# Optimization experiments

Hardware: AMD Instinct MI355X
Metric: run time of the kernel (lower is better)

The kernel has to match this reference:

```python
import jax, jax.numpy as jnp
import numpy as np

DIM = 1024
HEADS = 16
D_HEAD = 64
INNER = HEADS * D_HEAD  # 1024
CTX_DIM = 768
FF_INNER = 4 * DIM  # 4096
EPS = 1e-5
SCALE = D_HEAD ** -0.5


def _layer_norm(x, g, b):
    m = jnp.mean(x, axis=-1, keepdims=True)
    v = jnp.mean(jnp.square(x - m), axis=-1, keepdims=True)
    return (x - m) * jax.lax.rsqrt(v + EPS) * g + b


def _attention(x, ctx, wq, wk, wv, wo, bo):
    B, S, _ = x.shape
    T = ctx.shape[1]
    # project and split heads -> [B, H, S, Dh]
    q = (x @ wq).reshape(B, S, HEADS, D_HEAD).transpose(0, 2, 1, 3)
    k = (ctx @ wk).reshape(B, T, HEADS, D_HEAD).transpose(0, 2, 1, 3)
    v = (ctx @ wv).reshape(B, T, HEADS, D_HEAD).transpose(0, 2, 1, 3)
    attn = jnp.einsum('bhid,bhjd->bhij', q, k) * SCALE
    attn = jax.nn.softmax(attn, axis=-1)
    out = jnp.einsum('bhij,bhjd->bhid', attn, v)  # [B, H, S, Dh]
    out = out.transpose(0, 2, 1, 3).reshape(B, S, INNER)
    return out @ wo + bo


def setup_inputs() -> dict:
    key = jax.random.key(0)
    ks = jax.random.split(key, 20)
    rn = lambda k, shape, s=0.02: jax.random.normal(k, shape, dtype=jnp.float32) * s
    inp = {
        'hidden_states': jax.random.normal(ks[0], (4, 2048, DIM), dtype=jnp.float32),
        'context': jax.random.normal(ks[1], (4, 77, CTX_DIM), dtype=jnp.float32),
        # self-attention
        'wq1': rn(ks[2], (DIM, INNER)), 'wk1': rn(ks[3], (DIM, INNER)),
        'wv1': rn(ks[4], (DIM, INNER)),
        'wo1': rn(ks[5], (INNER, DIM)), 'bo1': jnp.zeros((DIM,), jnp.float32),
        # cross-attention (k/v from context dim 768)
        'wq2': rn(ks[6], (DIM, INNER)), 'wk2': rn(ks[7], (CTX_DIM, INNER)),
        'wv2': rn(ks[8], (CTX_DIM, INNER)),
        'wo2': rn(ks[9], (INNER, DIM)), 'bo2': jnp.zeros((DIM,), jnp.float32),
        # GEGLU feed-forward
        'w_ff1': rn(ks[10], (DIM, 2 * FF_INNER)), 'b_ff1': jnp.zeros((2 * FF_INNER,), jnp.float32),
        'w_ff2': rn(ks[11], (FF_INNER, DIM)), 'b_ff2': jnp.zeros((DIM,), jnp.float32),
        # layer norms
        'ln1_g': jnp.ones((DIM,), jnp.float32), 'ln1_b': jnp.zeros((DIM,), jnp.float32),
        'ln2_g': jnp.ones((DIM,), jnp.float32), 'ln2_b': jnp.zeros((DIM,), jnp.float32),
        'ln3_g': jnp.ones((DIM,), jnp.float32), 'ln3_b': jnp.zeros((DIM,), jnp.float32),
    }
    return inp


def reference(hidden_states, context, wq1, wk1, wv1, wo1, bo1,
              wq2, wk2, wv2, wo2, bo2, w_ff1, b_ff1, w_ff2, b_ff2,
              ln1_g, ln1_b, ln2_g, ln2_b, ln3_g, ln3_b):
    # self-attention, pre-norm residual
    h = hidden_states
    h = h + _attention(_layer_norm(h, ln1_g, ln1_b), _layer_norm(h, ln1_g, ln1_b),
                       wq1, wk1, wv1, wo1, bo1)
    # cross-attention
    h = h + _attention(_layer_norm(h, ln2_g, ln2_b), context,
                       wq2, wk2, wv2, wo2, bo2)
    # GEGLU feed-forward
    x = _layer_norm(h, ln3_g, ln3_b) @ w_ff1 + b_ff1
    lin, gate = jnp.split(x, 2, axis=2)
    h = h + (lin * jax.nn.gelu(gate)) @ w_ff2 + b_ff2
    return h
```

## Files before the change

### kernel.cpp

```cpp
#include <hip/hip_runtime.h>

#define DIMM 1024
#define NHEADS 16
#define DHEAD 64
#define BATCH 4
#define SEQ 2048
#define TCTX 77
#define CTXD 768
#define FFI 4096

typedef float f32x4 __attribute__((ext_vector_type(4)));
typedef __bf16 bf16x8 __attribute__((ext_vector_type(8)));

__device__ __forceinline__ float bf2f(unsigned short u){
  union { unsigned int i; float f; } c; c.i = ((unsigned int)u) << 16; return c.f;
}
__device__ __forceinline__ unsigned short f2bf(float f){
  union { float f; unsigned int i; } c; c.f = f;
  unsigned int i = c.i;
  return (unsigned short)((i + 0x7fffu + ((i >> 16) & 1u)) >> 16);
}
__device__ __forceinline__ void cp16(const unsigned short* g, unsigned short* l){
  __builtin_amdgcn_global_load_lds(
      (const __attribute__((address_space(1))) unsigned int*)g,
      (__attribute__((address_space(3))) unsigned int*)l, 16, 0, 0);
}

__global__ __launch_bounds__(256) void ln_kernel(const float* __restrict__ x,
                                                 const float* __restrict__ g,
                                                 const float* __restrict__ bb,
                                                 unsigned short* __restrict__ y)
{
  int row = blockIdx.x, tid = threadIdx.x;
  float4 raw = ((const float4*)(x + (size_t)row * DIMM))[tid];
  float v0 = raw.x, v1 = raw.y, v2 = raw.z, v3 = raw.w;
  float s  = v0 + v1 + v2 + v3;
  float sq = v0*v0 + v1*v1 + v2*v2 + v3*v3;
  #pragma unroll
  for (int off = 32; off; off >>= 1){ s += __shfl_xor(s, off); sq += __shfl_xor(sq, off); }
  __shared__ float sm[8];
  int wave = tid >> 6, lane = tid & 63;
  if (lane == 0){ sm[wave] = s; sm[4 + wave] = sq; }
  __syncthreads();
  s  = sm[0] + sm[1] + sm[2] + sm[3];
  sq = sm[4] + sm[5] + sm[6] + sm[7];
  float mean = s * (1.f / DIMM);
  float var  = sq * (1.f / DIMM) - mean * mean;
  float rstd = rsqrtf(var + 1e-5f);
  float4 gr = ((const float4*)g)[tid];
  float4 br = ((const float4*)bb)[tid];
  ushort4 o;
  o.x = f2bf((v0 - mean) * rstd * gr.x + br.x);
  o.y = f2bf((v1 - mean) * rstd * gr.y + br.y);
  o.z = f2bf((v2 - mean) * rstd * gr.z + br.z);
  o.w = f2bf((v3 - mean) * rstd * gr.w + br.w);
  ((ushort4*)(y + (size_t)row * DIMM))[tid] = o;
}

__global__ __launch_bounds__(256) void wt_kernel(const float* __restrict__ in,
                                                 unsigned short* __restrict__ out,
                                                 int K, int N)
{
  __shared__ float t[32][33];
  int tx = threadIdx.x & 31, ty = threadIdx.x >> 5;
  int k0 = blockIdx.y * 32, n0 = blockIdx.x * 32;
  #pragma unroll
  for (int i = 0; i < 4; i++)
    t[ty + i * 8][tx] = in[(size_t)(k0 + ty + i * 8) * N + n0 + tx];
  __syncthreads();
  #pragma unroll
  for (int i = 0; i < 4; i++)
    out[(size_t)(n0 + ty + i * 8) * K + k0 + tx] = f2bf(t[tx][ty + i * 8]);
}

#define CTXE (TCTX * BATCH * CTXD)
__global__ __launch_bounds__(256) void ctxcvt_kernel(const float* __restrict__ in,
                                                     unsigned short* __restrict__ out)
{
  int e = (blockIdx.x * 256 + threadIdx.x) * 4;
  float4 v;
  if (e < CTXE) v = *(const float4*)(in + e);
  else { v.x = 0.f; v.y = 0.f; v.z = 0.f; v.w = 0.f; }
  ushort4 o; o.x = f2bf(v.x); o.y = f2bf(v.y); o.z = f2bf(v.z); o.w = f2bf(v.w);
  *(ushort4*)(out + e) = o;
}

template<int RESF, int CF32>
__global__ __launch_bounds__(256) void gemm_bt(
    const unsigned short* __restrict__ A, int lda,
    const unsigned short* __restrict__ Bt, int ldb,
    const float* __restrict__ bias, const void* __restrict__ resv,
    void* __restrict__ Cv, int ldc,
    int M, int N, int K)
{
  __shared__ __align__(16) unsigned short As[128][64];
  __shared__ __align__(16) unsigned short Bs[128][64];
  int tid = threadIdx.x;
  int n0 = blockIdx.x * 128, row0 = blockIdx.y * 128;
  int wave = tid >> 6, lane = tid & 63, quad = lane >> 4, l16 = lane & 15;
  int wm = (wave >> 1) * 64, wn = (wave & 1) * 64;
  int wrow = wave * 32;
  int lrow = lane >> 3, lgrp = lane & 7;
  int gcol = ((lgrp ^ lrow) * 8);

  f32x4 acc[4][4];
  #pragma unroll
  for (int mt = 0; mt < 4; mt++)
    #pragma unroll
    for (int nt = 0; nt < 4; nt++) acc[mt][nt] = 0.f;

  for (int k0 = 0; k0 < K; k0 += 64) {
    const unsigned short* ga = A  + (size_t)(row0 + wrow + lrow) * lda + k0 + gcol;
    const unsigned short* gb = Bt + (size_t)(n0  + wrow + lrow) * ldb + k0 + gcol;
    #pragma unroll
    for (int i = 0; i < 4; i++){
      cp16(ga + (size_t)(8 * i) * lda, &As[wrow + 8 * i][0]);
      cp16(gb + (size_t)(8 * i) * ldb, &Bs[wrow + 8 * i][0]);
    }
    __syncthreads();
    #pragma unroll
    for (int kc = 0; kc < 2; kc++){
      bf16x8 af[4], bf[4];
      #pragma unroll
      for (int mt = 0; mt < 4; mt++){
        int R = wm + mt * 16 + l16;
        af[mt] = *(const bf16x8*)&As[R][((kc * 4 + quad) ^ (R & 7)) * 8];
      }
      #pragma unroll
      for (int nt = 0; nt < 4; nt++){
        int R = wn + nt * 16 + l16;
        bf[nt] = *(const bf16x8*)&Bs[R][((kc * 4 + quad) ^ (R & 7)) * 8];
      }
      #pragma unroll
      for (int mt = 0; mt < 4; mt++)
        #pragma unroll
        for (int nt = 0; nt < 4; nt++)
          acc[mt][nt] = __builtin_amdgcn_mfma_f32_16x16x32_bf16(af[mt], bf[nt], acc[mt][nt], 0, 0, 0);
    }
    __syncthreads();
  }

  #pragma unroll
  for (int nt = 0; nt < 4; nt++){
    int c = n0 + wn + nt * 16 + l16;
    float bv = bias ? bias[c] : 0.f;
    #pragma unroll
    for (int mt = 0; mt < 4; mt++){
      int rbase = row0 + wm + mt * 16 + quad * 4;
      #pragma unroll
      for (int rr = 0; rr < 4; rr++){
        int r = rbase + rr;
        if (r < M) {
          float val = acc[mt][nt][rr] + bv;
          size_t idx = (size_t)r * ldc + c;
          if (RESF) val += ((const float*)resv)[idx];
          if (CF32) ((float*)Cv)[idx] = val;
          else      ((unsigned short*)Cv)[idx] = f2bf(val);
        }
      }
    }
  }
}

__global__ __launch_bounds__(256) void ff1_geglu_bt(
    const unsigned short* __restrict__ A,
    const unsigned short* __restrict__ BtW,
    const float* __restrict__ bias,
    unsigned short* __restrict__ Z, int M)
{
  __shared__ __align__(16) unsigned short As[128][64];
  __shared__ __align__(16) unsigned short BsL[128][64];
  __shared__ __align__(16) unsigned short BsG[128][64];
  int tid = threadIdx.x;
  int n0 = blockIdx.x * 128, row0 = blockIdx.y * 128;
  int wave = tid >> 6, lane = tid & 63, quad = lane >> 4, l16 = lane & 15;
  int wm = (wave >> 1) * 64, wn = (wave & 1) * 64;
  int wrow = wave * 32;
  int lrow = lane >> 3, lgrp = lane & 7;
  int gcol = ((lgrp ^ lrow) * 8);

  f32x4 accL[4][4], accG[4][4];
  #pragma unroll
  for (int mt = 0; mt < 4; mt++)
    #pragma unroll
    for (int nt = 0; nt < 4; nt++){ accL[mt][nt] = 0.f; accG[mt][nt] = 0.f; }

  for (int k0 = 0; k0 < DIMM; k0 += 64) {
    const unsigned short* ga = A   + (size_t)(row0 + wrow + lrow) * DIMM + k0 + gcol;
    const unsigned short* gl = BtW + (size_t)(n0  + wrow + lrow) * DIMM + k0 + gcol;
    const unsigned short* gg = BtW + (size_t)(FFI + n0 + wrow + lrow) * DIMM + k0 + gcol;
    #pragma unroll
    for (int i = 0; i < 4; i++){
      cp16(ga + (size_t)(8 * i) * DIMM, &As[wrow + 8 * i][0]);
      cp16(gl + (size_t)(8 * i) * DIMM, &BsL[wrow + 8 * i][0]);
      cp16(gg + (size_t)(8 * i) * DIMM, &BsG[wrow + 8 * i][0]);
    }
    __syncthreads();
    #pragma unroll
    for (int kc = 0; kc < 2; kc++){
      bf16x8 af[4], b[4];
      #pragma unroll
      for (int mt = 0; mt < 4; mt++){
        int R = wm + mt * 16 + l16;
        af[mt] = *(const bf16x8*)&As[R][((kc * 4 + quad) ^ (R & 7)) * 8];
      }
      #pragma unroll
      for (int nt = 0; nt < 4; nt++){
        int R = wn + nt * 16 + l16;
        b[nt] = *(const bf16x8*)&BsL[R][((kc * 4 + quad) ^ (R & 7)) * 8];
      }
      #pragma unroll
      for (int mt = 0; mt < 4; mt++)
        #pragma unroll
        for (int nt = 0; nt < 4; nt++)
          accL[mt][nt] = __builtin_amdgcn_mfma_f32_16x16x32_bf16(af[mt], b[nt], accL[mt][nt], 0, 0, 0);
      #pragma unroll
      for (int nt = 0; nt < 4; nt++){
        int R = wn + nt * 16 + l16;
        b[nt] = *(const bf16x8*)&BsG[R][((kc * 4 + quad) ^ (R & 7)) * 8];
      }
      #pragma unroll
      for (int mt = 0; mt < 4; mt++)
        #pragma unroll
        for (int nt = 0; nt < 4; nt++)
          accG[mt][nt] = __builtin_amdgcn_mfma_f32_16x16x32_bf16(af[mt], b[nt], accG[mt][nt], 0, 0, 0);
    }
    __syncthreads();
  }

  #pragma unroll
  for (int nt = 0; nt < 4; nt++){
    int c = n0 + wn + nt * 16 + l16;
    float bvL = bias[c];
    float bvG = bias[c + FFI];
    #pragma unroll
    for (int mt = 0; mt < 4; mt++){
      int rbase = row0 + wm + mt * 16 + quad * 4;
      #pragma unroll
      for (int rr = 0; rr < 4; rr++){
        float lin = accL[mt][nt][rr] + bvL;
        float g   = accG[mt][nt][rr] + bvG;
        float y = 0.7978845608028654f * (g + 0.044715f * g * g * g);
        float e = __builtin_amdgcn_exp2f(y * 2.8853900817779268f);
        float t = 1.f - 2.f * __builtin_amdgcn_rcpf(e + 1.f);
        Z[(size_t)(rbase + rr) * FFI + c] = f2bf(lin * 0.5f * g * (1.f + t));
      }
    }
  }
}

__global__ __launch_bounds__(256, 8) void attn_mfma(
    const unsigned short* __restrict__ Q, int ldq,
    const unsigned short* __restrict__ Kb,
    const unsigned short* __restrict__ Vb, int ldkv,
    unsigned short* __restrict__ O,
    int S, int T, float scale)
{
  int tid = threadIdx.x, wave = tid >> 6, lane = tid & 63;
  int quad = lane >> 4, l16 = lane & 15;
  int bh = blockIdx.y, b = bh >> 4, h = bh & 15;
  int qw = blockIdx.x * 64 + wave * 16;

  __shared__ __align__(16) unsigned short Ks[64][64];
  __shared__ __align__(16) unsigned short Vt[64][72];

  float qs = scale * 1.44269504088896f;
  bf16x8 Qf[2];
  #pragma unroll
  for (int kc = 0; kc < 2; kc++){
    const unsigned short* qp = Q + ((size_t)b * S + qw + l16) * ldq
                                 + h * DHEAD + kc * 32 + quad * 8;
    union { float4 v; unsigned short u[8]; } ld; ld.v = *(const float4*)qp;
    union { bf16x8 v; unsigned short u[8]; } sc;
    #pragma unroll
    for (int j = 0; j < 8; j++) sc.u[j] = f2bf(bf2f(ld.u[j]) * qs);
    Qf[kc] = sc.v;
  }

  f32x4 Oacc[4];
  float lp = 0.f;
  #pragma unroll
  for (int nt = 0; nt < 4; nt++) Oacc[nt] = 0.f;

  int lrow = lane >> 3, lgrp = lane & 7;
  int gcol = (lgrp ^ lrow) * 8;

  for (int j0 = 0; j0 < T; j0 += 64){
    bool tail = (j0 + 64 > T);
    if (!tail){
      const unsigned short* gk = Kb + ((size_t)b * T + j0 + wave * 16 + lrow) * ldkv
                                    + h * DHEAD + gcol;
      cp16(gk,                      &Ks[wave * 16 + lrow][0]);
      cp16(gk + (size_t)8 * ldkv,   &Ks[wave * 16 + 8 + lrow][0]);
    } else {
      #pragma unroll
      for (int p = 0; p < 2; p++){
        int key = p * 32 + (tid >> 3);
        int g = tid & 7;
        float4 kv;
        if (j0 + key < T) kv = *(const float4*)(Kb + ((size_t)b * T + j0 + key) * ldkv + h * DHEAD + g * 8);
        else { kv.x = 0.f; kv.y = 0.f; kv.z = 0.f; kv.w = 0.f; }
        *(float4*)&Ks[key][(g ^ (key & 7)) * 8] = kv;
      }
    }
    {
      int j = tid & 63, dbs = (tid >> 6) * 16;
      if (j0 + j < T){
        union { float4 v; unsigned short u[8]; } v1, v2;
        const unsigned short* vp = Vb + ((size_t)b * T + j0 + j) * ldkv + h * DHEAD + dbs;
        v1.v = ((const float4*)vp)[0];
        v2.v = ((const float4*)vp)[1];
        #pragma unroll
        for (int u = 0; u < 8; u++){ Vt[dbs + u][j] = v1.u[u]; Vt[dbs + 8 + u][j] = v2.u[u]; }
      } else {
        #pragma unroll
        for (int u = 0; u < 8; u++){ Vt[dbs + u][j] = 0; Vt[dbs + 8 + u][j] = 0; }
      }
    }
    __syncthreads();

    union pfu { bf16x8 v; __bf16 e[8]; } pf[2];
    {
      f32x4 sT[4];
      #pragma unroll
      for (int nt = 0; nt < 4; nt++){
        sT[nt] = 0.f;
        #pragma unroll
        for (int kc = 0; kc < 2; kc++){
          bf16x8 kf = *(const bf16x8*)&Ks[nt * 16 + l16][((kc * 4 + quad) ^ (l16 & 7)) * 8];
          sT[nt] = __builtin_amdgcn_mfma_f32_16x16x32_bf16(kf, Qf[kc], sT[nt], 0, 0, 0);
        }
      }
      #pragma unroll
      for (int nt = 0; nt < 4; nt++)
        #pragma unroll
        for (int rr = 0; rr < 4; rr++){
          float sv = sT[nt][rr];
          if (tail && (j0 + nt * 16 + quad * 4 + rr) >= T) sv = -1e30f;
          float p = __builtin_amdgcn_exp2f(fminf(sv, 108.f));
          lp += p;
          pf[nt >> 1].e[(nt & 1) * 4 + rr] = (__bf16)p;
        }
    }

    #pragma unroll
    for (int kc = 0; kc < 2; kc++)
      #pragma unroll
      for (int nt = 0; nt < 4; nt++){
        union { bf16x8 v; ushort4 u[2]; } vf;
        vf.u[0] = *(const ushort4*)&Vt[nt * 16 + l16][kc * 32 + quad * 4];
        vf.u[1] = *(const ushort4*)&Vt[nt * 16 + l16][kc * 32 + 16 + quad * 4];
        Oacc[nt] = __builtin_amdgcn_mfma_f32_16x16x32_bf16(pf[kc].v, vf.v, Oacc[nt], 0, 0, 0);
      }
    __syncthreads();
  }

  float l = lp;
  l += __shfl_xor(l, 16);
  l += __shfl_xor(l, 32);
  float inv[4];
  #pragma unroll
  for (int rr = 0; rr < 4; rr++)
    inv[rr] = 1.f / __shfl(l, quad * 4 + rr);
  #pragma unroll
  for (int nt = 0; nt < 4; nt++)
    #pragma unroll
    for (int rr = 0; rr < 4; rr++){
      size_t idx = ((size_t)b * S + qw + quad * 4 + rr) * DIMM
                   + h * DHEAD + nt * 16 + l16;
      O[idx] = f2bf(Oacc[nt][rr] * inv[rr]);
    }
}

extern "C" void kernel_launch(void* const* d_in, const int* in_sizes, int n_in,
                              void* d_out, int out_size, void* d_ws, size_t ws_size,
                              hipStream_t stream)
{
  const float* h0   = (const float*)d_in[0];
  const float* ctx  = (const float*)d_in[1];
  const float* wq1  = (const float*)d_in[2];
  const float* wk1  = (const float*)d_in[3];
  const float* wv1  = (const float*)d_in[4];
  const float* wo1  = (const float*)d_in[5];
  const float* bo1  = (const float*)d_in[6];
  const float* wq2  = (const float*)d_in[7];
  const float* wk2  = (const float*)d_in[8];
  const float* wv2  = (const float*)d_in[9];
  const float* wo2  = (const float*)d_in[10];
  const float* bo2  = (const float*)d_in[11];
  const float* wff1 = (const float*)d_in[12];
  const float* bff1 = (const float*)d_in[13];
  const float* wff2 = (const float*)d_in[14];
  const float* bff2 = (const float*)d_in[15];
  const float* ln1g = (const float*)d_in[16];
  const float* ln1b = (const float*)d_in[17];
  const float* ln2g = (const float*)d_in[18];
  const float* ln2b = (const float*)d_in[19];
  const float* ln3g = (const float*)d_in[20];
  const float* ln3b = (const float*)d_in[21];

  unsigned short* wsp = (unsigned short*)d_ws;
  const size_t RD = (size_t)BATCH * SEQ * DIMM;
  unsigned short* xn  = wsp;
  unsigned short* qkv = wsp + RD;
  unsigned short* ar  = wsp + 4 * RD;
  unsigned short* zb  = qkv;
  float* hres = (float*)d_out;

  const size_t M1 = (size_t)1024 * 1024;
  const int ROWS = BATCH * SEQ;
  const int CROWS = BATCH * TCTX;
  const float scale = 0.125f;
  dim3 blk(256);
  dim3 attn_grid(SEQ / 64, BATCH * NHEADS);

  wt_kernel<<<dim3(32, 32), blk, 0, stream>>>(wq1, ar,          DIMM, DIMM);
  wt_kernel<<<dim3(32, 32), blk, 0, stream>>>(wk1, ar + M1,     DIMM, DIMM);
  wt_kernel<<<dim3(32, 32), blk, 0, stream>>>(wv1, ar + 2 * M1, DIMM, DIMM);
  wt_kernel<<<dim3(32, 32), blk, 0, stream>>>(wo1, ar + 3 * M1, DIMM, DIMM);
  ln_kernel<<<ROWS, blk, 0, stream>>>(h0, ln1g, ln1b, xn);
  gemm_bt<0,0><<<dim3(3072 / 128, ROWS / 128), blk, 0, stream>>>(
      xn, DIMM, ar, DIMM, nullptr, nullptr, qkv, 3072, ROWS, 3072, DIMM);
  attn_mfma<<<attn_grid, blk, 0, stream>>>(qkv, 3072, qkv + 1024, qkv + 2048, 3072, xn, SEQ, SEQ, scale);
  gemm_bt<1,1><<<dim3(DIMM / 128, ROWS / 128), blk, 0, stream>>>(
      xn, DIMM, ar + 3 * M1, DIMM, bo1, h0, hres, DIMM, ROWS, DIMM, DIMM);

  unsigned short* wq2T  = ar;
  unsigned short* wkv2T = ar + M1;
  unsigned short* wo2T  = ar + M1 + (size_t)2048 * CTXD;
  unsigned short* xc    = wo2T + M1;
  wt_kernel<<<dim3(32, 32), blk, 0, stream>>>(wq2, wq2T, DIMM, DIMM);
  wt_kernel<<<dim3(32, 24), blk, 0, stream>>>(wk2, wkv2T, CTXD, DIMM);
  wt_kernel<<<dim3(32, 24), blk, 0, stream>>>(wv2, wkv2T + (size_t)1024 * CTXD, CTXD, DIMM);
  wt_kernel<<<dim3(32, 32), blk, 0, stream>>>(wo2, wo2T, DIMM, DIMM);
  ctxcvt_kernel<<<(384 * CTXD / 4) / 256, blk, 0, stream>>>(ctx, xc);
  ln_kernel<<<ROWS, blk, 0, stream>>>(hres, ln2g, ln2b, xn);
  gemm_bt<0,0><<<dim3(DIMM / 128, ROWS / 128), blk, 0, stream>>>(
      xn, DIMM, wq2T, DIMM, nullptr, nullptr, qkv, DIMM, ROWS, DIMM, DIMM);
  unsigned short* kvc = qkv + RD;
  gemm_bt<0,0><<<dim3(2048 / 128, 3), blk, 0, stream>>>(
      xc, CTXD, wkv2T, CTXD, nullptr, nullptr, kvc, 2048, CROWS, 2048, CTXD);
  attn_mfma<<<attn_grid, blk, 0, stream>>>(qkv, 1024, kvc, kvc + 1024, 2048, xn, SEQ, TCTX, scale);
  gemm_bt<1,1><<<dim3(DIMM / 128, ROWS / 128), blk, 0, stream>>>(
      xn, DIMM, wo2T, DIMM, bo2, hres, hres, DIMM, ROWS, DIMM, DIMM);

  unsigned short* wff1T = ar;
  unsigned short* wff2T = ar + 8 * M1;
  wt_kernel<<<dim3(256, 32),  blk, 0, stream>>>(wff1, wff1T, DIMM, 2 * FFI);
  wt_kernel<<<dim3(32, 128),  blk, 0, stream>>>(wff2, wff2T, FFI, DIMM);
  ln_kernel<<<ROWS, blk, 0, stream>>>(hres, ln3g, ln3b, xn);
  for (int half = 0; half < 2; half++){
    int r0 = half * 4096;
    ff1_geglu_bt<<<dim3(FFI / 128, 4096 / 128), blk, 0, stream>>>(
        xn + (size_t)r0 * DIMM, wff1T, bff1, zb, 4096);
    gemm_bt<1,1><<<dim3(DIMM / 128, 4096 / 128), blk, 0, stream>>>(
        zb, FFI, wff2T, FFI, bff2, hres + (size_t)r0 * DIMM,
        hres + (size_t)r0 * DIMM, DIMM, 4096, DIMM, FFI);
  }
}
```

Measured before the change: 1.022 ms.

## Use 512-thread attention blocks and swizzled V layout for 128-byte fragment reads

The attention kernel now runs 8 waves per block over 128 queries, so each K/V tile loaded into shared memory serves twice as many query rows and per-thread load work halves. V is stored with an XOR-swizzled, MFMA-fragment-friendly layout, so each PV fragment becomes a single 16-byte LDS read instead of two 8-byte reads from a padded transpose. The risks are lower occupancy from larger blocks and that the cp16 destination passes only the row base, which relies on the global_load_lds lane-offset semantics.

```diff
diff --git a/kernel.cpp b/kernel.cpp
--- a/kernel.cpp
+++ b/kernel.cpp
@@ -249,7 +249,7 @@
   }
 }
 
-__global__ __launch_bounds__(256, 8) void attn_mfma(
+__global__ __launch_bounds__(512, 8) void attn_mfma(
     const unsigned short* __restrict__ Q, int ldq,
     const unsigned short* __restrict__ Kb,
     const unsigned short* __restrict__ Vb, int ldkv,
@@ -259,10 +259,10 @@
   int tid = threadIdx.x, wave = tid >> 6, lane = tid & 63;
   int quad = lane >> 4, l16 = lane & 15;
   int bh = blockIdx.y, b = bh >> 4, h = bh & 15;
-  int qw = blockIdx.x * 64 + wave * 16;
+  int qw = blockIdx.x * 128 + wave * 16;
 
   __shared__ __align__(16) unsigned short Ks[64][64];
-  __shared__ __align__(16) unsigned short Vt[64][72];
+  __shared__ __align__(16) unsigned short Vp[64][64];
 
   float qs = scale * 1.44269504088896f;
   bf16x8 Qf[2];
@@ -284,38 +284,31 @@
 
   int lrow = lane >> 3, lgrp = lane & 7;
   int gcol = (lgrp ^ lrow) * 8;
+  int vj = lane;
+  int vchunk = ((vj >> 5) << 2) | ((vj >> 2) & 3);
+  int velem  = (((vj >> 4) & 1) << 2) | (vj & 3);
+  int dbs = wave * 8;
 
   for (int j0 = 0; j0 < T; j0 += 64){
     bool tail = (j0 + 64 > T);
     if (!tail){
-      const unsigned short* gk = Kb + ((size_t)b * T + j0 + wave * 16 + lrow) * ldkv
+      const unsigned short* gk = Kb + ((size_t)b * T + j0 + wave * 8 + lrow) * ldkv
                                     + h * DHEAD + gcol;
-      cp16(gk,                      &Ks[wave * 16 + lrow][0]);
-      cp16(gk + (size_t)8 * ldkv,   &Ks[wave * 16 + 8 + lrow][0]);
+      cp16(gk, &Ks[wave * 8][0]);
     } else {
-      #pragma unroll
-      for (int p = 0; p < 2; p++){
-        int key = p * 32 + (tid >> 3);
-        int g = tid & 7;
-        float4 kv;
-        if (j0 + key < T) kv = *(const float4*)(Kb + ((size_t)b * T + j0 + key) * ldkv + h * DHEAD + g * 8);
-        else { kv.x = 0.f; kv.y = 0.f; kv.z = 0.f; kv.w = 0.f; }
-        *(float4*)&Ks[key][(g ^ (key & 7)) * 8] = kv;
-      }
+      int key = tid >> 3, g = tid & 7;
+      float4 kv;
+      if (j0 + key < T) kv = *(const float4*)(Kb + ((size_t)b * T + j0 + key) * ldkv + h * DHEAD + g * 8);
+      else { kv.x = 0.f; kv.y = 0.f; kv.z = 0.f; kv.w = 0.f; }
+      *(float4*)&Ks[key][(g ^ (key & 7)) * 8] = kv;
     }
     {
-      int j = tid & 63, dbs = (tid >> 6) * 16;
-      if (j0 + j < T){
-        union { float4 v; unsigned short u[8]; } v1, v2;
-        const unsigned short* vp = Vb + ((size_t)b * T + j0 + j) * ldkv + h * DHEAD + dbs;
-        v1.v = ((const float4*)vp)[0];
-        v2.v = ((const float4*)vp)[1];
-        #pragma unroll
-        for (int u = 0; u < 8; u++){ Vt[dbs + u][j] = v1.u[u]; Vt[dbs + 8 + u][j] = v2.u[u]; }
-      } else {
-        #pragma unroll
-        for (int u = 0; u < 8; u++){ Vt[dbs + u][j] = 0; Vt[dbs + 8 + u][j] = 0; }
-      }
+      union { float4 v; unsigned short u[8]; } vv;
+      if (j0 + vj < T) vv.v = *(const float4*)(Vb + ((size_t)b * T + j0 + vj) * ldkv + h * DHEAD + dbs);
+      else { vv.v.x = 0.f; vv.v.y = 0.f; vv.v.z = 0.f; vv.v.w = 0.f; }
+      #pragma unroll
+      for (int u = 0; u < 8; u++)
+        Vp[dbs + u][((vchunk ^ u) << 3) | velem] = vv.u[u];
     }
     __syncthreads();
 
@@ -347,10 +340,9 @@
     for (int kc = 0; kc < 2; kc++)
       #pragma unroll
       for (int nt = 0; nt < 4; nt++){
-        union { bf16x8 v; ushort4 u[2]; } vf;
-        vf.u[0] = *(const ushort4*)&Vt[nt * 16 + l16][kc * 32 + quad * 4];
-        vf.u[1] = *(const ushort4*)&Vt[nt * 16 + l16][kc * 32 + 16 + quad * 4];
-        Oacc[nt] = __builtin_amdgcn_mfma_f32_16x16x32_bf16(pf[kc].v, vf.v, Oacc[nt], 0, 0, 0);
+        int R = nt * 16 + l16;
+        bf16x8 vf = *(const bf16x8*)&Vp[R][((kc * 4 + quad) ^ (R & 7)) * 8];
+        Oacc[nt] = __builtin_amdgcn_mfma_f32_16x16x32_bf16(pf[kc].v, vf, Oacc[nt], 0, 0, 0);
       }
     __syncthreads();
   }
@@ -412,7 +404,8 @@
   const int CROWS = BATCH * TCTX;
   const float scale = 0.125f;
   dim3 blk(256);
-  dim3 attn_grid(SEQ / 64, BATCH * NHEADS);
+  dim3 ablk(512);
+  dim3 attn_grid(SEQ / 128, BATCH * NHEADS);
 
   wt_kernel<<<dim3(32, 32), blk, 0, stream>>>(wq1, ar,          DIMM, DIMM);
   wt_kernel<<<dim3(32, 32), blk, 0, stream>>>(wk1, ar + M1,     DIMM, DIMM);
@@ -421,7 +414,7 @@
   ln_kernel<<<ROWS, blk, 0, stream>>>(h0, ln1g, ln1b, xn);
   gemm_bt<0,0><<<dim3(3072 / 128, ROWS / 128), blk, 0, stream>>>(
       xn, DIMM, ar, DIMM, nullptr, nullptr, qkv, 3072, ROWS, 3072, DIMM);
-  attn_mfma<<<attn_grid, blk, 0, stream>>>(qkv, 3072, qkv + 1024, qkv + 2048, 3072, xn, SEQ, SEQ, scale);
+  attn_mfma<<<attn_grid, ablk, 0, stream>>>(qkv, 3072, qkv + 1024, qkv + 2048, 3072, xn, SEQ, SEQ, scale);
   gemm_bt<1,1><<<dim3(DIMM / 128, ROWS / 128), blk, 0, stream>>>(
       xn, DIMM, ar + 3 * M1, DIMM, bo1, h0, hres, DIMM, ROWS, DIMM, DIMM);
 
@@ -440,7 +433,7 @@
   unsigned short* kvc = qkv + RD;
   gemm_bt<0,0><<<dim3(2048 / 128, 3), blk, 0, stream>>>(
       xc, CTXD, wkv2T, CTXD, nullptr, nullptr, kvc, 2048, CROWS, 2048, CTXD);
-  attn_mfma<<<attn_grid, blk, 0, stream>>>(qkv, 1024, kvc, kvc + 1024, 2048, xn, SEQ, TCTX, scale);
+  attn_mfma<<<attn_grid, ablk, 0, stream>>>(qkv, 1024, kvc, kvc + 1024, 2048, xn, SEQ, TCTX, scale);
   gemm_bt<1,1><<<dim3(DIMM / 128, ROWS / 128), blk, 0, stream>>>(
       xn, DIMM, wo2T, DIMM, bo2, hres, hres, DIMM, ROWS, DIMM, DIMM);
 
```

Result: no change. 1.032 ms (+1.0%).
